# Performance work log

Hardware: AMD Instinct MI355X
Metric: run time of the kernel (lower is better)

Reference implementation:

```python
import jax, jax.numpy as jnp
import numpy as np

DECAY = 0.5
COEFF = 0.05
INH_C = 2.0
SPARSE_THRES = 0.9


def setup_inputs() -> dict:
    key = jax.random.key(0)
    k1, k2 = jax.random.split(key)
    x = jax.random.normal(k1, (1, 512, 448, 448), dtype=jnp.float32)
    # small-magnitude boost weights (buffer starts at zero in torch but we
    # use nonzero values so the mv / inhibition path is exercised)
    boost_weight = jax.random.normal(k2, (512, 512), dtype=jnp.float32) * 0.01
    return {"x": x, "boost_weight": boost_weight}


def reference(x, boost_weight):
    # x: [1, C, H, W]; boost_weight: [C, C]
    x_avr = jnp.mean(x[0], axis=(1, 2))                      # [C] adaptive avgpool(1) + squeeze
    boost_vec = boost_weight @ x_avr                          # [C]
    inh_value = jnp.mean(boost_vec)
    x_tmp = jax.nn.relu(x_avr + boost_vec - INH_C * inh_value)
    threshold = jnp.max(x_tmp) * SPARSE_THRES
    x_sparse = jnp.where(x_tmp < threshold, 0.0, x_tmp)      # masked_fill

    # Hebbian update (torch commit_update, done under no_grad):
    weight_tmp = jnp.outer(x_tmp, x_sparse)                  # [C, C]
    C = weight_tmp.shape[0]
    weight_tmp = weight_tmp * (1.0 - jnp.eye(C, dtype=weight_tmp.dtype))  # fill_diagonal_(0)
    norm = jnp.linalg.norm(weight_tmp)
    weight_tmp = jnp.where(
        jnp.isfinite(norm) & (norm > 0), weight_tmp / norm, weight_tmp
    )
    new_boost_weight = boost_weight * DECAY + COEFF * weight_tmp

    # gated channel rescale of the full tensor
    scale = (x_tmp / (x_avr + 1e-12)).reshape(1, -1, 1, 1)
    out = x * scale                                          # [1, C, H, W]
    return out, new_boost_weight
```

## Files before the change

### kernel.cpp

```cpp
#include <hip/hip_runtime.h>
#include <math.h>

#define NCH   512
#define HW    200704
#define HW4   50176
#define X_ELEMS 102760448ULL


__global__ __launch_bounds__(512) void k_channel_mean(const float* __restrict__ x,
                                                      float* __restrict__ ws) {
    __shared__ float red[8];
    const int c = blockIdx.x;
    const float4* xv = reinterpret_cast<const float4*>(x) + (size_t)c * HW4;
    float s = 0.f;
    #pragma unroll 4
    for (int i = threadIdx.x; i < HW4; i += 512) {
        float4 v = xv[i];
        s += (v.x + v.y) + (v.z + v.w);
    }
    #pragma unroll
    for (int o = 32; o > 0; o >>= 1) s += __shfl_down(s, o, 64);
    const int wave = threadIdx.x >> 6;
    const int lane = threadIdx.x & 63;
    if (lane == 0) red[wave] = s;
    __syncthreads();
    if (threadIdx.x == 0) {
        float t = 0.f;
        #pragma unroll
        for (int w = 0; w < 8; ++w) t += red[w];
        ws[c] = t * (1.0f / (float)HW);
    }
}

__global__ __launch_bounds__(512) void k_stats(const float* __restrict__ W,
                                               float* __restrict__ ws) {
    __shared__ float avr[512];
    __shared__ float red[8];
    __shared__ float redA[8], redB[8], redD[8];
    __shared__ float bcast;

    const int t = threadIdx.x;
    const int wave = t >> 6;
    const int lane = t & 63;

    avr[t] = ws[t];
    __syncthreads();

    float acc = 0.f;
    const float* row = W + (size_t)t * NCH;
    #pragma unroll 8
    for (int j = 0; j < NCH; ++j) acc += row[j] * avr[j];

    float s = acc;
    #pragma unroll
    for (int o = 32; o > 0; o >>= 1) s += __shfl_down(s, o, 64);
    if (lane == 0) red[wave] = s;
    __syncthreads();
    if (t == 0) {
        float tt = 0.f;
        #pragma unroll
        for (int w = 0; w < 8; ++w) tt += red[w];
        bcast = tt * (1.0f / (float)NCH);
    }
    __syncthreads();
    const float inh = bcast;

    float xtmp = avr[t] + acc - 2.0f * inh;
    xtmp = xtmp > 0.f ? xtmp : 0.f;

    float m = xtmp;
    #pragma unroll
    for (int o = 32; o > 0; o >>= 1) m = fmaxf(m, __shfl_down(m, o, 64));
    __syncthreads();
    if (lane == 0) red[wave] = m;
    __syncthreads();
    if (t == 0) {
        float mm = red[0];
        #pragma unroll
        for (int w = 1; w < 8; ++w) mm = fmaxf(mm, red[w]);
        bcast = mm * 0.9f;
    }
    __syncthreads();
    const float thr = bcast;
    const float xs = (xtmp < thr) ? 0.f : xtmp;

    float a = xtmp * xtmp;
    float b = xs * xs;
    float d = xtmp * xs; d = d * d;
    #pragma unroll
    for (int o = 32; o > 0; o >>= 1) {
        a += __shfl_down(a, o, 64);
        b += __shfl_down(b, o, 64);
        d += __shfl_down(d, o, 64);
    }
    if (lane == 0) { redA[wave] = a; redB[wave] = b; redD[wave] = d; }
    __syncthreads();
    if (t == 0) {
        float s1 = 0.f, s2 = 0.f, s3 = 0.f;
        #pragma unroll
        for (int w = 0; w < 8; ++w) { s1 += redA[w]; s2 += redB[w]; s3 += redD[w]; }
        float n2 = s1 * s2 - s3;
        float norm = (n2 > 0.f) ? sqrtf(n2) : 0.f;
        float inv = (norm > 0.f && isfinite(norm)) ? (1.0f / norm) : 1.0f;
        ws[2048] = inv;
    }

    ws[512 + t]  = xtmp;
    ws[1024 + t] = xs;
    ws[1536 + t] = xtmp / (avr[t] + 1e-12f);
}

__global__ __launch_bounds__(256) void k_weight_update(const float* __restrict__ W,
                                                       const float* __restrict__ ws,
                                                       float* __restrict__ outW) {
    const int idx = blockIdx.x * 256 + threadIdx.x;
    const int i = idx >> 9;
    const int j = idx & (NCH - 1);
    const float inv = ws[2048];
    const float v = (i == j) ? 0.f : ws[512 + i] * ws[1024 + j] * inv;
    outW[idx] = 0.5f * W[idx] + 0.05f * v;
}

__global__ __launch_bounds__(256) void k_scale(const float* __restrict__ x,
                                               const float* __restrict__ ws,
                                               float* __restrict__ out) {
    const int c = blockIdx.y;
    const float s = ws[1536 + c];
    const size_t chan_base = (size_t)c * HW4;
    const int base = blockIdx.x * 1024 + threadIdx.x;
    const float4* xv = reinterpret_cast<const float4*>(x);
    float4* ov = reinterpret_cast<float4*>(out);
    #pragma unroll
    for (int k = 0; k < 4; ++k) {
        const size_t off = chan_base + (size_t)(base + k * 256);
        float4 v = xv[off];
        v.x *= s; v.y *= s; v.z *= s; v.w *= s;
        ov[off] = v;
    }
}

extern "C" void kernel_launch(void* const* d_in, const int* in_sizes, int n_in,
                              void* d_out, int out_size, void* d_ws, size_t ws_size,
                              hipStream_t stream) {
    const float* x = (const float*)d_in[0];
    const float* W = (const float*)d_in[1];
    float* out  = (float*)d_out;
    float* outW = out + X_ELEMS;
    float* ws   = (float*)d_ws;

    k_channel_mean<<<NCH, 512, 0, stream>>>(x, ws);
    k_stats<<<1, 512, 0, stream>>>(W, ws);
    k_weight_update<<<(NCH * NCH) / 256, 256, 0, stream>>>(W, ws, outW);
    dim3 grid_scale(49, NCH);
    k_scale<<<grid_scale, 256, 0, stream>>>(x, ws, out);
}
```

Baseline: 774.6 us.

## Split channel mean across groups, fuse tail kernels, reverse channel order, nontemporal stores

The channel mean is now computed by 8 partial blocks per channel, with k_stats summing the partials, which puts more blocks in flight during the first pass. The weight update and the scale pass are merged into a single kernel launch. The scale pass walks channels in reverse order so the most recently read channels, likely still in cache, are scaled first, and it writes its output with nontemporal stores so the written data does not evict x from cache. This adds a small extra reduction step and changes the workspace layout.

After: 757.5 us. 2.2% less time.

```diff
diff --git a/kernel.cpp b/kernel.cpp
--- a/kernel.cpp
+++ b/kernel.cpp
@@ -1,20 +1,28 @@
 #include <hip/hip_runtime.h>
 #include <math.h>
 
-#define NCH   512
-#define HW    200704
-#define HW4   50176
+#define NCH    512
+#define HW     200704
+#define HW4    50176
+#define GROUPS 8
+#define G4     6272
 #define X_ELEMS 102760448ULL
 
+#define WS_XTMP  4096
+#define WS_XSP   4608
+#define WS_SCALE 5120
+#define WS_INV   5632
 
-__global__ __launch_bounds__(512) void k_channel_mean(const float* __restrict__ x,
+typedef float vf4 __attribute__((ext_vector_type(4)));
+
+__global__ __launch_bounds__(256) void k_mean_partial(const float* __restrict__ x,
                                                       float* __restrict__ ws) {
-    __shared__ float red[8];
-    const int c = blockIdx.x;
-    const float4* xv = reinterpret_cast<const float4*>(x) + (size_t)c * HW4;
+    __shared__ float red[4];
+    const int g = blockIdx.x;
+    const int c = blockIdx.y;
+    const float4* xv = reinterpret_cast<const float4*>(x) + (size_t)c * HW4 + (size_t)g * G4;
     float s = 0.f;
-    #pragma unroll 4
-    for (int i = threadIdx.x; i < HW4; i += 512) {
+    for (int i = threadIdx.x; i < G4; i += 256) {
         float4 v = xv[i];
         s += (v.x + v.y) + (v.z + v.w);
     }
@@ -25,10 +33,7 @@
     if (lane == 0) red[wave] = s;
     __syncthreads();
     if (threadIdx.x == 0) {
-        float t = 0.f;
-        #pragma unroll
-        for (int w = 0; w < 8; ++w) t += red[w];
-        ws[c] = t * (1.0f / (float)HW);
+        ws[g * NCH + c] = (red[0] + red[1]) + (red[2] + red[3]);
     }
 }
 
@@ -43,7 +48,12 @@
     const int wave = t >> 6;
     const int lane = t & 63;
 
-    avr[t] = ws[t];
+    {
+        float s = 0.f;
+        #pragma unroll
+        for (int g = 0; g < GROUPS; ++g) s += ws[g * NCH + t];
+        avr[t] = s * (1.0f / (float)HW);
+    }
     __syncthreads();
 
     float acc = 0.f;
@@ -102,40 +112,44 @@
         float n2 = s1 * s2 - s3;
         float norm = (n2 > 0.f) ? sqrtf(n2) : 0.f;
         float inv = (norm > 0.f && isfinite(norm)) ? (1.0f / norm) : 1.0f;
-        ws[2048] = inv;
+        ws[WS_INV] = inv;
     }
 
-    ws[512 + t]  = xtmp;
-    ws[1024 + t] = xs;
-    ws[1536 + t] = xtmp / (avr[t] + 1e-12f);
+    ws[WS_XTMP + t]  = xtmp;
+    ws[WS_XSP + t]   = xs;
+    ws[WS_SCALE + t] = xtmp / (avr[t] + 1e-12f);
 }
 
-__global__ __launch_bounds__(256) void k_weight_update(const float* __restrict__ W,
-                                                       const float* __restrict__ ws,
-                                                       float* __restrict__ outW) {
-    const int idx = blockIdx.x * 256 + threadIdx.x;
-    const int i = idx >> 9;
-    const int j = idx & (NCH - 1);
-    const float inv = ws[2048];
-    const float v = (i == j) ? 0.f : ws[512 + i] * ws[1024 + j] * inv;
-    outW[idx] = 0.5f * W[idx] + 0.05f * v;
-}
-
-__global__ __launch_bounds__(256) void k_scale(const float* __restrict__ x,
-                                               const float* __restrict__ ws,
-                                               float* __restrict__ out) {
-    const int c = blockIdx.y;
-    const float s = ws[1536 + c];
-    const size_t chan_base = (size_t)c * HW4;
-    const int base = blockIdx.x * 1024 + threadIdx.x;
-    const float4* xv = reinterpret_cast<const float4*>(x);
-    float4* ov = reinterpret_cast<float4*>(out);
-    #pragma unroll
-    for (int k = 0; k < 4; ++k) {
-        const size_t off = chan_base + (size_t)(base + k * 256);
-        float4 v = xv[off];
-        v.x *= s; v.y *= s; v.z *= s; v.w *= s;
-        ov[off] = v;
+__global__ __launch_bounds__(256) void k_tail(const float* __restrict__ x,
+                                              const float* __restrict__ W,
+                                              const float* __restrict__ ws,
+                                              float* __restrict__ out,
+                                              float* __restrict__ outW) {
+    const int bid = blockIdx.x;
+    if (bid < 1024) {
+        const int idx = bid * 256 + threadIdx.x;
+        const int i = idx >> 9;
+        const int j = idx & (NCH - 1);
+        const float inv = ws[WS_INV];
+        const float v = (i == j) ? 0.f : ws[WS_XTMP + i] * ws[WS_XSP + j] * inv;
+        outW[idx] = 0.5f * W[idx] + 0.05f * v;
+    } else {
+        const int b = bid - 1024;
+        const int c_lin = b / 49;
+        const int t = b - c_lin * 49;
+        const int c = (NCH - 1) - c_lin;
+        const float s = ws[WS_SCALE + c];
+        const size_t chan_base = (size_t)c * HW4;
+        const int base = t * 1024 + threadIdx.x;
+        const float4* xv = reinterpret_cast<const float4*>(x);
+        float4* ov = reinterpret_cast<float4*>(out);
+        #pragma unroll
+        for (int k = 0; k < 4; ++k) {
+            const size_t off = chan_base + (size_t)(base + k * 256);
+            float4 v = xv[off];
+            v.x *= s; v.y *= s; v.z *= s; v.w *= s;
+            __builtin_nontemporal_store(*(const vf4*)&v, (vf4*)&ov[off]);
+        }
     }
 }
 
@@ -148,9 +162,8 @@
     float* outW = out + X_ELEMS;
     float* ws   = (float*)d_ws;
 
-    k_channel_mean<<<NCH, 512, 0, stream>>>(x, ws);
+    dim3 grid_mean(GROUPS, NCH);
+    k_mean_partial<<<grid_mean, 256, 0, stream>>>(x, ws);
     k_stats<<<1, 512, 0, stream>>>(W, ws);
-    k_weight_update<<<(NCH * NCH) / 256, 256, 0, stream>>>(W, ws, outW);
-    dim3 grid_scale(49, NCH);
-    k_scale<<<grid_scale, 256, 0, stream>>>(x, ws, out);
+    k_tail<<<1024 + 49 * NCH, 256, 0, stream>>>(x, W, ws, out, outW);
 }
```
